# Kernel tuning notes

Hardware: AMD Instinct MI355X
Metric: run time of the kernel (lower is better)

## Reference

```python
import jax, jax.numpy as jnp
import numpy as np

B, N, C, OUT, E = 8, 16384, 128, 256, 262144


def setup_inputs() -> dict:
    key = jax.random.key(0)
    k1, k2, k3 = jax.random.split(key, 3)
    x = jax.random.normal(k1, (B, N, C), dtype=jnp.float32)
    edge_index = jax.random.randint(k2, (2, E), 0, N, dtype=jnp.int64)
    W = jax.random.normal(k3, (C, OUT), dtype=jnp.float32) * 0.02
    b = jnp.zeros((OUT,), dtype=jnp.float32)
    return {"x": x, "edge_index": edge_index, "W": W, "b": b}


def reference(x, edge_index, W, b):
    # x: (B, N, C); edge_index: (2, E) shared across the batch (as in the torch code,
    # which repeats row/col B times with batch offsets -> equivalent to per-batch segment max).
    row, col = edge_index[0], edge_index[1]
    n = x.shape[1]

    def agg_one(xb):  # xb: (N, C)
        x_j = xb[col]  # gather neighbor features, (E, C)
        a = jax.ops.segment_max(x_j, row, num_segments=n)  # amax scatter-reduce
        # nodes with no incoming edge: torch fills -1e9 then zeros them; segment_max gives -inf
        return jnp.where(jnp.isfinite(a), a, 0.0)

    aggr = jax.vmap(agg_one)(x) - x  # max-relative: max_j(x_j) - x_i, (B, N, C)
    h = jnp.einsum("bnc,co->bno", aggr, W) + b
    return jax.nn.gelu(h, approximate=False)  # torch nn.GELU() is exact erf GELU
```

## Files before the change

kernel.cpp:

```cpp
#include <hip/hip_runtime.h>
#include <hip/hip_bf16.h>

#define B_   8
#define N_   16384
#define C_   128
#define OUT_ 256
#define E_   262144

#define CNT_OFF  0u
#define OVFC_OFF 16384u
#define OVF_OFF  16448u
#define TAB_OFF  540736u
#define WT_OFF   1589312u
#define XBF_OFF  1605696u

typedef __attribute__((ext_vector_type(8))) short bf16x8;
typedef __attribute__((ext_vector_type(4))) float f32x4;

__device__ __forceinline__ unsigned short f2bf(float f) {
  unsigned u = __float_as_uint(f);
  u += 0x7FFFu + ((u >> 16) & 1u);
  return (unsigned short)(u >> 16);
}
__device__ __forceinline__ float gelu_exact(float v) {
  return 0.5f * v * (1.0f + erff(v * 0.70710678118654752f));
}
__device__ __forceinline__ unsigned umin_(unsigned a, unsigned b) {
  return a < b ? a : b;
}

__global__ __launch_bounds__(256) void k_prep(const float* __restrict__ x,
                                              const unsigned* __restrict__ eidx,
                                              const float* __restrict__ W,
                                              unsigned* __restrict__ ws) {
  const unsigned bid = blockIdx.x, tid = threadIdx.x;
  if (bid < 16384u) {
    unsigned i = bid * 256u + tid;
    float4 v = ((const float4*)x)[i];
    uint2 o;
    o.x = (unsigned)f2bf(v.x) | ((unsigned)f2bf(v.y) << 16);
    o.y = (unsigned)f2bf(v.z) | ((unsigned)f2bf(v.w) << 16);
    ((uint2*)(ws + XBF_OFF))[i] = o;
  } else if (bid < 17408u) {
    __shared__ int flag32;
    if (tid == 0) flag32 = 0;
    __syncthreads();
    unsigned e = (bid - 16384u) * 256u + tid;
    if (eidx[2u * e + 1u] != 0u) flag32 = 1;
    __syncthreads();
    int row, col;
    if (flag32) {
      row = (int)eidx[e];
      col = (int)eidx[e + E_];
    } else {
      const long long* p = (const long long*)eidx;
      row = (int)p[e];
      col = (int)p[e + E_];
    }
    unsigned pos = atomicAdd(ws + CNT_OFF + (unsigned)row, 1u);
    if (pos < 64u) {
      ws[TAB_OFF + ((unsigned)row << 6) + pos] = (unsigned)col;
    } else {
      unsigned o = atomicAdd(ws + OVFC_OFF, 1u);
      ws[OVF_OFF + 2u * o]      = (unsigned)row;
      ws[OVF_OFF + 2u * o + 1u] = (unsigned)col;
    }
  } else {
    unsigned t = (bid - 17408u) * 256u + tid;
    unsigned n = t >> 7, k = t & 127u;
    ((unsigned short*)(ws + WT_OFF))[n * 128u + k] = f2bf(W[k * 256u + n]);
  }
}

__global__ __launch_bounds__(256, 4) void k_ag(const uint4* __restrict__ xbf4,
                                               const unsigned* __restrict__ ws,
                                               const unsigned short* __restrict__ Wt,
                                               const float* __restrict__ bias,
                                               float* __restrict__ out) {
  __shared__ unsigned short sm[128 * 136];
  const unsigned bi = blockIdx.x;
  const unsigned b  = bi & 7u;
  const unsigned mbase = (bi >> 3) << 6;
  const unsigned tid = threadIdx.x;
  const unsigned wv = tid >> 6;
  const unsigned lane = tid & 63u;
  const unsigned g  = lane >> 4;
  const unsigned ln = lane & 15u;
  const uint4* xb = xbf4 + ((size_t)b << 18);
  const unsigned wbase = mbase + (wv << 4);

#define MAXU4(U, ml, mh)                                                    \
  mh[0] = fmaxf(mh[0], __uint_as_float((U).x));                             \
  ml[0] = fmaxf(ml[0], __uint_as_float((U).x << 16));                       \
  mh[1] = fmaxf(mh[1], __uint_as_float((U).y));                             \
  ml[1] = fmaxf(ml[1], __uint_as_float((U).y << 16));                       \
  mh[2] = fmaxf(mh[2], __uint_as_float((U).z));                             \
  ml[2] = fmaxf(ml[2], __uint_as_float((U).z << 16));                       \
  mh[3] = fmaxf(mh[3], __uint_as_float((U).w));                             \
  ml[3] = fmaxf(ml[3], __uint_as_float((U).w << 16));

  for (unsigned i = 0u; i < 16u; i += 2u) {
    const unsigned ra = wbase + i, rb = ra + 1u;
    const unsigned dega = ws[CNT_OFF + ra];
    const unsigned degb = ws[CNT_OFF + rb];
    const unsigned d64a = dega < 64u ? dega : 64u;
    const unsigned d64b = degb < 64u ? degb : 64u;
    const unsigned dm1a = d64a - 1u;
    const unsigned dm1b = d64b - 1u;
    const unsigned tva = ws[TAB_OFF + (ra << 6) + lane];
    const unsigned tvb = ws[TAB_OFF + (rb << 6) + lane];
    const unsigned cprea = dega ? tva : ra;
    const unsigned cpreb = degb ? tvb : rb;
    const uint4 xwa = xb[((size_t)ra << 4) + ln];
    const uint4 xwb = xb[((size_t)rb << 4) + ln];

    float mloa[4], mhia[4], mlob[4], mhib[4];
#pragma unroll
    for (int r = 0; r < 4; ++r) {
      mloa[r] = -INFINITY; mhia[r] = -INFINITY;
      mlob[r] = -INFINITY; mhib[r] = -INFINITY;
    }

    if (dega | degb) {
      const unsigned mx = d64a > d64b ? d64a : d64b;
      for (unsigned t = 0u; t < mx; t += 16u) {
        unsigned ca[4], cb[4];
#pragma unroll
        for (int k = 0; k < 4; ++k) {
          unsigned e = t + 4u * (unsigned)k + g;
          ca[k] = (unsigned)__shfl((int)cprea, (int)umin_(umin_(e, dm1a), 63u));
          cb[k] = (unsigned)__shfl((int)cpreb, (int)umin_(umin_(e, dm1b), 63u));
        }
        uint4 ua[4], ub[4];
#pragma unroll
        for (int k = 0; k < 4; ++k) ua[k] = xb[((size_t)ca[k] << 4) + ln];
#pragma unroll
        for (int k = 0; k < 4; ++k) ub[k] = xb[((size_t)cb[k] << 4) + ln];
#pragma unroll
        for (int k = 0; k < 4; ++k) { MAXU4(ua[k], mloa, mhia) }
#pragma unroll
        for (int k = 0; k < 4; ++k) { MAXU4(ub[k], mlob, mhib) }
      }
    }
    if ((dega > 64u) | (degb > 64u)) {
      unsigned no = ws[OVFC_OFF];
      for (unsigned k2 = g; k2 < no; k2 += 4u) {
        unsigned rr = ws[OVF_OFF + 2u * k2];
        if (rr == ra) {
          uint4 u = xb[((size_t)ws[OVF_OFF + 2u * k2 + 1u] << 4) + ln];
          MAXU4(u, mloa, mhia)
        } else if (rr == rb) {
          uint4 u = xb[((size_t)ws[OVF_OFF + 2u * k2 + 1u] << 4) + ln];
          MAXU4(u, mlob, mhib)
        }
      }
    }

#pragma unroll
    for (int r = 0; r < 4; ++r) {
      mloa[r] = fmaxf(mloa[r], __shfl_xor(mloa[r], 16, 64));
      mhia[r] = fmaxf(mhia[r], __shfl_xor(mhia[r], 16, 64));
      mloa[r] = fmaxf(mloa[r], __shfl_xor(mloa[r], 32, 64));
      mhia[r] = fmaxf(mhia[r], __shfl_xor(mhia[r], 32, 64));
      mlob[r] = fmaxf(mlob[r], __shfl_xor(mlob[r], 16, 64));
      mhib[r] = fmaxf(mhib[r], __shfl_xor(mhib[r], 16, 64));
      mlob[r] = fmaxf(mlob[r], __shfl_xor(mlob[r], 32, 64));
      mhib[r] = fmaxf(mhib[r], __shfl_xor(mhib[r], 32, 64));
    }

    if (g == 0u) {
      const bool hasa = (dega != 0u), hasb = (degb != 0u);
      unsigned xva[4] = {xwa.x, xwa.y, xwa.z, xwa.w};
      unsigned xvb[4] = {xwb.x, xwb.y, xwb.z, xwb.w};
      unsigned oxa[4], oxb[4];
#pragma unroll
      for (int r = 0; r < 4; ++r) {
        float vloa = hasa ? mloa[r] : 0.0f;
        float vhia = hasa ? __uint_as_float(__float_as_uint(mhia[r]) & 0xFFFF0000u) : 0.0f;
        oxa[r] = (unsigned)f2bf(vloa - __uint_as_float(xva[r] << 16)) |
                 ((unsigned)f2bf(vhia - __uint_as_float(xva[r] & 0xFFFF0000u)) << 16);
        float vlob = hasb ? mlob[r] : 0.0f;
        float vhib = hasb ? __uint_as_float(__float_as_uint(mhib[r]) & 0xFFFF0000u) : 0.0f;
        oxb[r] = (unsigned)f2bf(vlob - __uint_as_float(xvb[r] << 16)) |
                 ((unsigned)f2bf(vhib - __uint_as_float(xvb[r] & 0xFFFF0000u)) << 16);
      }
      uint4 oa = {oxa[0], oxa[1], oxa[2], oxa[3]};
      uint4 ob = {oxb[0], oxb[1], oxb[2], oxb[3]};
      *(uint4*)&sm[wv * 2176u + i * 136u + ln * 8u]        = oa;
      *(uint4*)&sm[wv * 2176u + (i + 1u) * 136u + ln * 8u] = ob;
    }
  }
#undef MAXU4

  __syncthreads();

  const unsigned q = g;
  bf16x8 af[4];
#pragma unroll
  for (int kc = 0; kc < 4; ++kc)
    af[kc] = *(const bf16x8*)&sm[wv * 2176u + ln * 136u + (unsigned)kc * 32u + q * 8u];
  __syncthreads();

#pragma unroll
  for (int half = 0; half < 2; ++half) {
    const int nbase = half * 128;
#pragma unroll
    for (int i = 0; i < 8; ++i) {
      int slot = i * 256 + (int)tid;
      int n = slot >> 4, k8 = slot & 15;
      uint4 u = *(const uint4*)(Wt + (size_t)(nbase + n) * 128 + k8 * 8);
      *(uint4*)&sm[n * 136 + k8 * 8] = u;
    }
    __syncthreads();

    f32x4 acc[8];
#pragma unroll
    for (int f = 0; f < 8; ++f) acc[f] = (f32x4){0.f, 0.f, 0.f, 0.f};
#pragma unroll
    for (int kc = 0; kc < 4; ++kc) {
#pragma unroll
      for (int f = 0; f < 8; ++f) {
        bf16x8 bf = *(const bf16x8*)&sm[(f * 16 + (int)ln) * 136 + kc * 32 + (int)q * 8];
        acc[f] = __builtin_amdgcn_mfma_f32_16x16x32_bf16(af[kc], bf, acc[f], 0, 0, 0);
      }
    }

#pragma unroll
    for (int f = 0; f < 8; ++f) {
      int n = nbase + f * 16 + (int)ln;
      float bv = bias[n];
#pragma unroll
      for (int r = 0; r < 4; ++r) {
        unsigned mrow = ((size_t)b << 14) + mbase + (wv << 4) + q * 4u + (unsigned)r;
        out[(size_t)mrow * 256 + n] = gelu_exact(acc[f][r] + bv);
      }
    }
    __syncthreads();
  }
}

extern "C" void kernel_launch(void* const* d_in, const int* in_sizes, int n_in,
                              void* d_out, int out_size, void* d_ws, size_t ws_size,
                              hipStream_t stream) {
  const float* x      = (const float*)d_in[0];
  const unsigned* eid = (const unsigned*)d_in[1];
  const float* W      = (const float*)d_in[2];
  const float* bia    = (const float*)d_in[3];
  float* out          = (float*)d_out;
  unsigned* ws        = (unsigned*)d_ws;

  const unsigned short* Wt = (const unsigned short*)(ws + WT_OFF);

  hipMemsetAsync(ws + CNT_OFF, 0, 16448 * sizeof(unsigned), stream);
  hipLaunchKernelGGL(k_prep, dim3(17536), dim3(256), 0, stream, x, eid, W, ws);
  hipLaunchKernelGGL(k_ag,   dim3(2048),  dim3(256), 0, stream,
                     (const uint4*)(ws + XBF_OFF), ws, Wt, bia, out);
}
```

Baseline: 284.6 us.

## Halve LDS tile for higher occupancy, split per-row gather loops, nontemporal I/O

The shared-memory buffer shrinks to 64x136 so more blocks can fit per CU, and launch bounds rise to 8 blocks per CU. To fit, the GEMM stage now loads W in four 64-column quarters instead of two 128-column halves. The gather loop handles the two rows separately, so a low-degree row no longer issues redundant clamped loads while the other row still has edges. Per-row degrees are fetched once per wave and broadcast with shuffles. Table loads and output stores become nontemporal. The trade-off is twice as many W reload and barrier rounds in the GEMM stage, plus tighter register limits at the higher occupancy.

```diff
diff --git a/kernel.cpp b/kernel.cpp
--- a/kernel.cpp
+++ b/kernel.cpp
@@ -72,12 +72,12 @@
   }
 }
 
-__global__ __launch_bounds__(256, 4) void k_ag(const uint4* __restrict__ xbf4,
+__global__ __launch_bounds__(256, 8) void k_ag(const uint4* __restrict__ xbf4,
                                                const unsigned* __restrict__ ws,
                                                const unsigned short* __restrict__ Wt,
                                                const float* __restrict__ bias,
                                                float* __restrict__ out) {
-  __shared__ unsigned short sm[128 * 136];
+  __shared__ unsigned short sm[8704];
   const unsigned bi = blockIdx.x;
   const unsigned b  = bi & 7u;
   const unsigned mbase = (bi >> 3) << 6;
@@ -89,6 +89,8 @@
   const uint4* xb = xbf4 + ((size_t)b << 18);
   const unsigned wbase = mbase + (wv << 4);
 
+  const unsigned cnt16 = ws[CNT_OFF + wbase + ln];
+
 #define MAXU4(U, ml, mh)                                                    \
   mh[0] = fmaxf(mh[0], __uint_as_float((U).x));                             \
   ml[0] = fmaxf(ml[0], __uint_as_float((U).x << 16));                       \
@@ -101,16 +103,14 @@
 
   for (unsigned i = 0u; i < 16u; i += 2u) {
     const unsigned ra = wbase + i, rb = ra + 1u;
-    const unsigned dega = ws[CNT_OFF + ra];
-    const unsigned degb = ws[CNT_OFF + rb];
+    const unsigned dega = (unsigned)__shfl((int)cnt16, (int)i);
+    const unsigned degb = (unsigned)__shfl((int)cnt16, (int)(i + 1u));
     const unsigned d64a = dega < 64u ? dega : 64u;
     const unsigned d64b = degb < 64u ? degb : 64u;
     const unsigned dm1a = d64a - 1u;
     const unsigned dm1b = d64b - 1u;
-    const unsigned tva = ws[TAB_OFF + (ra << 6) + lane];
-    const unsigned tvb = ws[TAB_OFF + (rb << 6) + lane];
-    const unsigned cprea = dega ? tva : ra;
-    const unsigned cpreb = degb ? tvb : rb;
+    const unsigned cprea = __builtin_nontemporal_load(ws + TAB_OFF + (ra << 6) + lane);
+    const unsigned cpreb = __builtin_nontemporal_load(ws + TAB_OFF + (rb << 6) + lane);
     const uint4 xwa = xb[((size_t)ra << 4) + ln];
     const uint4 xwb = xb[((size_t)rb << 4) + ln];
 
@@ -121,23 +121,29 @@
       mlob[r] = -INFINITY; mhib[r] = -INFINITY;
     }
 
-    if (dega | degb) {
-      const unsigned mx = d64a > d64b ? d64a : d64b;
-      for (unsigned t = 0u; t < mx; t += 16u) {
-        unsigned ca[4], cb[4];
-#pragma unroll
-        for (int k = 0; k < 4; ++k) {
-          unsigned e = t + 4u * (unsigned)k + g;
-          ca[k] = (unsigned)__shfl((int)cprea, (int)umin_(umin_(e, dm1a), 63u));
-          cb[k] = (unsigned)__shfl((int)cpreb, (int)umin_(umin_(e, dm1b), 63u));
-        }
-        uint4 ua[4], ub[4];
+    const unsigned mx = d64a > d64b ? d64a : d64b;
+    for (unsigned t = 0u; t < mx; t += 16u) {
+      if (t < d64a) {
+        unsigned ca[4];
+#pragma unroll
+        for (int k = 0; k < 4; ++k)
+          ca[k] = (unsigned)__shfl((int)cprea,
+                                   (int)umin_(t + 4u * (unsigned)k + g, dm1a));
+        uint4 ua[4];
 #pragma unroll
         for (int k = 0; k < 4; ++k) ua[k] = xb[((size_t)ca[k] << 4) + ln];
 #pragma unroll
+        for (int k = 0; k < 4; ++k) { MAXU4(ua[k], mloa, mhia) }
+      }
+      if (t < d64b) {
+        unsigned cb[4];
+#pragma unroll
+        for (int k = 0; k < 4; ++k)
+          cb[k] = (unsigned)__shfl((int)cpreb,
+                                   (int)umin_(t + 4u * (unsigned)k + g, dm1b));
+        uint4 ub[4];
+#pragma unroll
         for (int k = 0; k < 4; ++k) ub[k] = xb[((size_t)cb[k] << 4) + ln];
-#pragma unroll
-        for (int k = 0; k < 4; ++k) { MAXU4(ua[k], mloa, mhia) }
 #pragma unroll
         for (int k = 0; k < 4; ++k) { MAXU4(ub[k], mlob, mhib) }
       }
@@ -145,7 +151,7 @@
     if ((dega > 64u) | (degb > 64u)) {
       unsigned no = ws[OVFC_OFF];
       for (unsigned k2 = g; k2 < no; k2 += 4u) {
-        unsigned rr = ws[OVF_OFF + 2u * k2];
+        unsigned rr = __builtin_nontemporal_load(ws + OVF_OFF + 2u * k2);
         if (rr == ra) {
           uint4 u = xb[((size_t)ws[OVF_OFF + 2u * k2 + 1u] << 4) + ln];
           MAXU4(u, mloa, mhia)
@@ -202,37 +208,38 @@
   __syncthreads();
 
 #pragma unroll
-  for (int half = 0; half < 2; ++half) {
-    const int nbase = half * 128;
-#pragma unroll
-    for (int i = 0; i < 8; ++i) {
-      int slot = i * 256 + (int)tid;
+  for (int qt = 0; qt < 4; ++qt) {
+    const int nbase = qt * 64;
+#pragma unroll
+    for (int i2 = 0; i2 < 4; ++i2) {
+      int slot = i2 * 256 + (int)tid;
       int n = slot >> 4, k8 = slot & 15;
       uint4 u = *(const uint4*)(Wt + (size_t)(nbase + n) * 128 + k8 * 8);
       *(uint4*)&sm[n * 136 + k8 * 8] = u;
     }
     __syncthreads();
 
-    f32x4 acc[8];
-#pragma unroll
-    for (int f = 0; f < 8; ++f) acc[f] = (f32x4){0.f, 0.f, 0.f, 0.f};
+    f32x4 acc[4];
+#pragma unroll
+    for (int f = 0; f < 4; ++f) acc[f] = (f32x4){0.f, 0.f, 0.f, 0.f};
 #pragma unroll
     for (int kc = 0; kc < 4; ++kc) {
 #pragma unroll
-      for (int f = 0; f < 8; ++f) {
+      for (int f = 0; f < 4; ++f) {
         bf16x8 bf = *(const bf16x8*)&sm[(f * 16 + (int)ln) * 136 + kc * 32 + (int)q * 8];
         acc[f] = __builtin_amdgcn_mfma_f32_16x16x32_bf16(af[kc], bf, acc[f], 0, 0, 0);
       }
     }
 
 #pragma unroll
-    for (int f = 0; f < 8; ++f) {
+    for (int f = 0; f < 4; ++f) {
       int n = nbase + f * 16 + (int)ln;
       float bv = bias[n];
 #pragma unroll
       for (int r = 0; r < 4; ++r) {
-        unsigned mrow = ((size_t)b << 14) + mbase + (wv << 4) + q * 4u + (unsigned)r;
-        out[(size_t)mrow * 256 + n] = gelu_exact(acc[f][r] + bv);
+        size_t mrow = ((size_t)b << 14) + mbase + (wv << 4) + q * 4u + (unsigned)r;
+        __builtin_nontemporal_store(gelu_exact(acc[f][r] + bv),
+                                    &out[mrow * 256 + n]);
       }
     }
     __syncthreads();
```

New measurement: 317.4 us. 11.5% more time.
